# Performance work log

Measured on AMD Instinct MI355X. Metric: run time of the kernel, lower is better.

## Reference

```python
import jax, jax.numpy as jnp
import numpy as np

N = 8000        # nodes
E = 64000       # directed edges (before self-loops)
F_IN = 3201     # node_dim=1 + encoding_dim(128)*25
N_TRAIN = 4000


def setup_inputs() -> dict:
    key = jax.random.key(0)
    k = jax.random.split(key, 4)
    d = {
        'x': jax.random.normal(k[0], (N, F_IN), dtype=jnp.float32),
        'edge_index': jax.random.randint(k[1], (2, E), 0, N),
        'y': jax.random.uniform(k[2], (N,), dtype=jnp.float32),
        'train_idx': jax.random.randint(k[3], (N_TRAIN,), 0, N),
    }
    cnt = [0]
    def w(shape, fan_in):
        cnt[0] += 1
        kk = jax.random.fold_in(jax.random.key(1), cnt[0])
        return (jax.random.normal(kk, shape, dtype=jnp.float32) / np.float32(np.sqrt(fan_in)))
    ones = lambda n: jnp.ones((n,), jnp.float32)
    zeros = lambda n: jnp.zeros((n,), jnp.float32)
    d['bn0_g'] = ones(F_IN); d['bn0_b'] = zeros(F_IN)
    d['W1l'] = w((F_IN, 1024), F_IN); d['W1r'] = w((F_IN, 1024), F_IN)
    d['a1'] = w((2, 512), 512); d['b1'] = zeros(1024)
    d['bn1_g'] = ones(1024); d['bn1_b'] = zeros(1024)
    d['W2l'] = w((1024, 512), 1024); d['W2r'] = w((1024, 512), 1024)
    d['a2'] = w((1, 512), 512); d['b2'] = zeros(512)
    d['bn2_g'] = ones(512); d['bn2_b'] = zeros(512)
    d['W3l'] = w((512, 512), 512); d['W3r'] = w((512, 512), 512)
    d['a3'] = w((1, 512), 512); d['b3'] = zeros(512)
    d['bn3_g'] = ones(512); d['bn3_b'] = zeros(512)
    d['W4l'] = w((512, 512), 512); d['W4r'] = w((512, 512), 512)
    d['a4'] = w((1, 512), 512); d['b4'] = zeros(512)
    d['Wh'] = w((512, 1), 512); d['bh'] = zeros(1)
    return d


def _batchnorm(h, g, b, eps=1e-5):
    # training-mode batch statistics over the node dim
    m = h.mean(axis=0)
    v = h.var(axis=0)
    return (h - m) * jax.lax.rsqrt(v + jnp.float32(eps)) * g + b


def _gatv2(h, src, dst, Wl, Wr, att, bias, n):
    # GATv2Conv with concat heads, softmax over incoming edges, aggr='mean'
    H, C = att.shape
    xl = (h @ Wl).reshape(n, H, C)   # source transform
    xr = (h @ Wr).reshape(n, H, C)   # target transform
    z = jax.nn.leaky_relu(xl[src] + xr[dst], negative_slope=0.2)  # [E,H,C]
    e = jnp.einsum('ehc,hc->eh', z, att)                          # [E,H]
    emax = jax.ops.segment_max(e, dst, num_segments=n)            # segment softmax
    ex = jnp.exp(e - emax[dst])
    denom = jax.ops.segment_sum(ex, dst, num_segments=n)
    alpha = ex / denom[dst]
    agg = jax.ops.segment_sum(alpha[:, :, None] * xl[src], dst, num_segments=n)
    deg = jax.ops.segment_sum(jnp.ones(src.shape[0], h.dtype), dst, num_segments=n)
    return (agg / deg[:, None, None]).reshape(n, H * C) + bias


def reference(x, edge_index, y, train_idx, bn0_g, bn0_b, W1l, W1r, a1, b1,
              bn1_g, bn1_b, W2l, W2r, a2, b2, bn2_g, bn2_b, W3l, W3r, a3, b3,
              bn3_g, bn3_b, W4l, W4r, a4, b4, Wh, bh):
    n = x.shape[0]
    loops = jnp.arange(n, dtype=edge_index.dtype)  # PyG add_self_loops=True
    src = jnp.concatenate([edge_index[0], loops])
    dst = jnp.concatenate([edge_index[1], loops])
    h = _batchnorm(x, bn0_g, bn0_b)
    h = _gatv2(h, src, dst, W1l, W1r, a1, b1, n)          # -> [N,1024]
    h = jax.nn.relu(_batchnorm(h, bn1_g, bn1_b))
    h = _gatv2(h, src, dst, W2l, W2r, a2, b2, n)          # -> [N,512]
    h = jax.nn.relu(_batchnorm(h, bn2_g, bn2_b))
    h = _gatv2(h, src, dst, W3l, W3r, a3, b3, n)
    h = jax.nn.relu(_batchnorm(h, bn3_g, bn3_b))
    h = jax.nn.relu(_gatv2(h, src, dst, W4l, W4r, a4, b4, n))
    pred = jax.nn.sigmoid(h @ Wh + bh)[:, 0]              # [N]
    return pred[train_idx], y[train_idx]
```

## Files before the change

kernel.cpp:

```cpp
#include <hip/hip_runtime.h>
#include <math.h>

typedef __bf16 bf16x8 __attribute__((ext_vector_type(8)));
typedef float f32x4 __attribute__((ext_vector_type(4)));
typedef unsigned short ushort8 __attribute__((ext_vector_type(8)));

__device__ __forceinline__ float bf2f(unsigned short u) {
  union { unsigned int i; float f; } c; c.i = ((unsigned int)u) << 16; return c.f;
}
__device__ __forceinline__ unsigned short f2bf(float f) {
  union { float f; unsigned int i; } c; c.f = f;
  unsigned int r = (c.i + 0x7fffu + ((c.i >> 16) & 1u)) >> 16;
  return (unsigned short)r;
}

__global__ void zero_k(float* __restrict__ statz, int nz, int* __restrict__ deg, int n) {
  int i = blockIdx.x * blockDim.x + threadIdx.x;
  if (i < nz) statz[i] = 0.f;
  if (i < n) deg[i] = 1;
}

__global__ void deg_count_k(const int* __restrict__ dst, int* __restrict__ deg, int e) {
  int i = blockIdx.x * blockDim.x + threadIdx.x;
  if (i < e) atomicAdd(&deg[dst[i]], 1);
}

__global__ void scan_k(const int* __restrict__ deg, int* __restrict__ offsets,
                       int* __restrict__ cursor, int n) {
  __shared__ int sums[1024];
  int tid = threadIdx.x;
  int chunk = (n + 1023) >> 10;
  int base = tid * chunk;
  int s = 0;
  for (int i = 0; i < chunk; ++i) {
    int j = base + i;
    if (j < n) s += deg[j];
  }
  sums[tid] = s;
  __syncthreads();
  for (int off = 1; off < 1024; off <<= 1) {
    int v = (tid >= off) ? sums[tid - off] : 0;
    __syncthreads();
    sums[tid] += v;
    __syncthreads();
  }
  int run = sums[tid] - s;
  for (int i = 0; i < chunk; ++i) {
    int j = base + i;
    if (j < n) {
      offsets[j] = run;
      cursor[j] = run;
      run += deg[j];
    }
  }
  if (tid == 1023) offsets[n] = sums[1023];
}

__global__ void csr_fill_k(const int* __restrict__ src, const int* __restrict__ dst,
                           int* __restrict__ cursor, int* __restrict__ csr_src,
                           int e, int n) {
  int i = blockIdx.x * blockDim.x + threadIdx.x;
  if (i >= e + n) return;
  int s, d;
  if (i < e) { s = src[i]; d = dst[i]; }
  else       { s = i - e;  d = s; }
  int pos = atomicAdd(&cursor[d], 1);
  csr_src[pos] = s;
}

__global__ __launch_bounds__(256)
void stats_convert_k(const float* __restrict__ x, unsigned short* __restrict__ Abf,
                     float* __restrict__ s1, float* __restrict__ s2,
                     int M, int K, int Kp) {
  int c = blockIdx.x * 256 + threadIdx.x;
  if (c >= Kp) return;
  int rows = (M + gridDim.y - 1) / gridDim.y;
  int r0 = blockIdx.y * rows;
  int r1 = min(M, r0 + rows);
  if (c >= K) {
    for (int r = r0; r < r1; ++r) Abf[(size_t)r * Kp + c] = 0;
    return;
  }
  float a = 0.f, b = 0.f;
  int r = r0;
  for (; r + 4 <= r1; r += 4) {
    float v0 = x[(size_t)(r + 0) * K + c];
    float v1 = x[(size_t)(r + 1) * K + c];
    float v2 = x[(size_t)(r + 2) * K + c];
    float v3 = x[(size_t)(r + 3) * K + c];
    a += v0 + v1 + v2 + v3;
    b += v0 * v0 + v1 * v1 + v2 * v2 + v3 * v3;
    Abf[(size_t)(r + 0) * Kp + c] = f2bf(v0);
    Abf[(size_t)(r + 1) * Kp + c] = f2bf(v1);
    Abf[(size_t)(r + 2) * Kp + c] = f2bf(v2);
    Abf[(size_t)(r + 3) * Kp + c] = f2bf(v3);
  }
  for (; r < r1; ++r) {
    float v = x[(size_t)r * K + c];
    a += v; b += v * v;
    Abf[(size_t)r * Kp + c] = f2bf(v);
  }
  atomicAdd(&s1[c], a);
  atomicAdd(&s2[c], b);
}

__global__ __launch_bounds__(256)
void col_stats_bf_k(const unsigned short* __restrict__ h, int M, int D,
                    float* __restrict__ s1, float* __restrict__ s2) {
  int c = blockIdx.x * 256 + threadIdx.x;
  if (c >= D) return;
  int rows = (M + gridDim.y - 1) / gridDim.y;
  int r0 = blockIdx.y * rows;
  int r1 = min(M, r0 + rows);
  float a = 0.f, b = 0.f;
  int r = r0;
  for (; r + 4 <= r1; r += 4) {
    float v0 = bf2f(h[(size_t)(r + 0) * D + c]);
    float v1 = bf2f(h[(size_t)(r + 1) * D + c]);
    float v2 = bf2f(h[(size_t)(r + 2) * D + c]);
    float v3 = bf2f(h[(size_t)(r + 3) * D + c]);
    a += v0 + v1 + v2 + v3;
    b += v0 * v0 + v1 * v1 + v2 * v2 + v3 * v3;
  }
  for (; r < r1; ++r) {
    float v = bf2f(h[(size_t)r * D + c]);
    a += v; b += v * v;
  }
  atomicAdd(&s1[c], a);
  atomicAdd(&s2[c], b);
}

__global__ void bn_fin_k(const float* __restrict__ s1, const float* __restrict__ s2,
                         const float* __restrict__ g, const float* __restrict__ b,
                         float* __restrict__ acol, float* __restrict__ ccol,
                         int D, float invM) {
  int c = blockIdx.x * blockDim.x + threadIdx.x;
  if (c >= D) return;
  float m = s1[c] * invM;
  float v = fmaxf(s2[c] * invM - m * m, 0.f);
  float a = rsqrtf(v + 1e-5f) * g[c];
  acol[c] = a;
  ccol[c] = b[c] - m * a;
}

__global__ __launch_bounds__(256)
void bn_apply8_k(const unsigned short* __restrict__ h,
                 const float* __restrict__ s1, const float* __restrict__ s2,
                 const float* __restrict__ g, const float* __restrict__ b,
                 unsigned short* __restrict__ outb,
                 size_t total, int D, float invM) {
  size_t i = ((size_t)blockIdx.x * 256 + threadIdx.x) * 8;
  if (i >= total) return;
  ushort8 u = *(const ushort8*)(h + i);
  int c = (int)(i % (size_t)D);
  ushort8 o;
#pragma unroll
  for (int j = 0; j < 8; ++j) {
    float m = s1[c + j] * invM;
    float var = fmaxf(s2[c + j] * invM - m * m, 0.f);
    float a = rsqrtf(var + 1e-5f) * g[c + j];
    float cc = b[c + j] - m * a;
    float v = bf2f(u[j]) * a + cc;
    o[j] = f2bf(fmaxf(v, 0.f));
  }
  *(ushort8*)(outb + i) = o;
}

__global__ __launch_bounds__(256)
void wconv_pair_k(const float* __restrict__ Wl, const float* __restrict__ Wr,
                  unsigned short* __restrict__ WT, int K, int N, int Kp,
                  const float* __restrict__ scale, const float* __restrict__ cshift,
                  float* __restrict__ bias) {
  const float* W = blockIdx.z ? Wr : Wl;
  unsigned short* WTo = WT + (size_t)blockIdx.z * N * Kp;
  __shared__ float t[32][33];
  int n0 = blockIdx.x * 32, k0 = blockIdx.y * 32;
  int tx = threadIdx.x & 31, ty = threadIdx.x >> 5;
  float bsum = 0.f;
#pragma unroll
  for (int i = 0; i < 32; i += 8) {
    int k = k0 + ty + i, nn = n0 + tx;
    float v = (k < K && nn < N) ? W[(size_t)k * N + nn] : 0.f;
    t[ty + i][tx] = v;
    if (cshift && k < K) bsum += cshift[k] * v;
  }
  if (cshift) atomicAdd(&bias[blockIdx.z * N + n0 + tx], bsum);
  __syncthreads();
#pragma unroll
  for (int i = 0; i < 32; i += 8) {
    int nn = n0 + ty + i, k = k0 + tx;
    if (nn < N && k < Kp) {
      float v = t[tx][ty + i];
      if (scale && k < K) v *= scale[k];
      WTo[(size_t)nn * Kp + k] = f2bf(v);
    }
  }
}

__global__ __launch_bounds__(256)
void gemm_bf16_k(const unsigned short* __restrict__ A,
                 const unsigned short* __restrict__ Bt,
                 unsigned short* __restrict__ outL, unsigned short* __restrict__ outR,
                 const float* __restrict__ bias, int M, int Nh, int K) {
  __shared__ unsigned short sA[128 * 64];
  __shared__ unsigned short sB[128 * 64];
  const int tid = threadIdx.x;
  const int wave = tid >> 6, lane = tid & 63;
  const int wm = wave >> 1, wn = wave & 1;
  const int l16 = lane & 15, lq = lane >> 4;
  const int row0 = blockIdx.y * 128, col0 = blockIdx.x * 128;

  f32x4 acc[4][4] = {};

  for (int kt = 0; kt < K; kt += 64) {
#pragma unroll
    for (int i = 0; i < 4; ++i) {
      int s = i * 256 + tid;
      int r = s >> 3;
      int g = (s & 7) ^ (r & 7);
      int ra = row0 + r;
      ra = ra < M ? ra : M - 1;
      const unsigned short* ga = A + (size_t)ra * K + (kt + g * 8);
      __builtin_amdgcn_global_load_lds(
          (const __attribute__((address_space(1))) void*)ga,
          (__attribute__((address_space(3))) void*)&sA[s * 8], 16, 0, 0);
      const unsigned short* gb = Bt + (size_t)(col0 + r) * K + (kt + g * 8);
      __builtin_amdgcn_global_load_lds(
          (const __attribute__((address_space(1))) void*)gb,
          (__attribute__((address_space(3))) void*)&sB[s * 8], 16, 0, 0);
    }
    __syncthreads();
#pragma unroll
    for (int ks = 0; ks < 2; ++ks) {
      bf16x8 af[4], bff[4];
#pragma unroll
      for (int t = 0; t < 4; ++t) {
        int g = ks * 4 + lq;
        int r = wm * 64 + t * 16 + l16;
        af[t] = *(const bf16x8*)&sA[(r * 8 + (g ^ (r & 7))) * 8];
        int rb = wn * 64 + t * 16 + l16;
        bff[t] = *(const bf16x8*)&sB[(rb * 8 + (g ^ (rb & 7))) * 8];
      }
#pragma unroll
      for (int mt = 0; mt < 4; ++mt)
#pragma unroll
        for (int nt = 0; nt < 4; ++nt)
          acc[mt][nt] = __builtin_amdgcn_mfma_f32_16x16x32_bf16(af[mt], bff[nt], acc[mt][nt], 0, 0, 0);
    }
    __syncthreads();
  }
#pragma unroll
  for (int mt = 0; mt < 4; ++mt) {
    int rbase = row0 + wm * 64 + mt * 16 + lq * 4;
#pragma unroll
    for (int nt = 0; nt < 4; ++nt) {
      int col = col0 + wn * 64 + nt * 16 + l16;
      float bv = bias ? bias[col] : 0.f;
      unsigned short* base;
      int cc;
      if (col < Nh) { base = outL; cc = col; }
      else          { base = outR; cc = col - Nh; }
#pragma unroll
      for (int r = 0; r < 4; ++r) {
        int rr = rbase + r;
        if (rr < M) base[(size_t)rr * Nh + cc] = f2bf(acc[mt][nt][r] + bv);
      }
    }
  }
}

template <int H>
__global__ __launch_bounds__(256)
void gat_edge_k(const unsigned short* __restrict__ xl, const unsigned short* __restrict__ xr,
                const float* __restrict__ att, const float* __restrict__ bias,
                const int* __restrict__ csr, const int* __restrict__ offsets,
                unsigned short* __restrict__ out, int n, int relu) {
  int gw = (blockIdx.x * 256 + threadIdx.x) >> 6;
  int lane = threadIdx.x & 63;
  if (gw >= n * H) return;
  int node, head;
  if (H == 1) { node = gw; head = 0; }
  else        { node = gw >> 1; head = gw & 1; }
  const int W = H * 512;
  const size_t rowoff = (size_t)node * W + head * 512;
  const size_t choff = (size_t)head * 512 + (size_t)(lane * 8);

  float xrv[8], atv[8];
  {
    ushort8 u = *(const ushort8*)(xr + rowoff + lane * 8);
    const float* ap = att + head * 512 + lane * 8;
#pragma unroll
    for (int j = 0; j < 8; ++j) { xrv[j] = bf2f(u[j]); atv[j] = ap[j]; }
  }
  int p0 = offsets[node], p1 = offsets[node + 1];
  ushort8 u0 = *(const ushort8*)(xl + (size_t)csr[p0] * W + choff);
  ushort8 u1 = u0;
  if (p0 + 1 < p1) u1 = *(const ushort8*)(xl + (size_t)csr[p0 + 1] * W + choff);

  float m = -1e30f, l = 0.f;
  float acc[8];
#pragma unroll
  for (int j = 0; j < 8; ++j) acc[j] = 0.f;
  for (int p = p0; p < p1; ++p) {
    ushort8 u = u0;
    u0 = u1;
    if (p + 2 < p1) u1 = *(const ushort8*)(xl + (size_t)csr[p + 2] * W + choff);
    float lv[8];
    float e = 0.f;
#pragma unroll
    for (int j = 0; j < 8; ++j) {
      lv[j] = bf2f(u[j]);
      float z = lv[j] + xrv[j];
      z = fmaxf(z, 0.f) + 0.2f * fminf(z, 0.f);
      e = fmaf(z, atv[j], e);
    }
#pragma unroll
    for (int off = 32; off > 0; off >>= 1) e += __shfl_xor(e, off, 64);
    float mn = fmaxf(m, e);
    float corr = __expf(m - mn);
    float w = __expf(e - mn);
    l = l * corr + w;
#pragma unroll
    for (int j = 0; j < 8; ++j) acc[j] = acc[j] * corr + w * lv[j];
    m = mn;
  }
  float inv = 1.f / (l * (float)(p1 - p0));
  const float* bp = bias + head * 512 + lane * 8;
  ushort8 o;
#pragma unroll
  for (int j = 0; j < 8; ++j) {
    float v = acc[j] * inv + bp[j];
    if (relu) v = fmaxf(v, 0.f);
    o[j] = f2bf(v);
  }
  *(ushort8*)(out + rowoff + lane * 8) = o;
}

__global__ __launch_bounds__(256)
void head_gather_k(const unsigned short* __restrict__ h, const float* __restrict__ Wh,
                   const float* __restrict__ bh, const float* __restrict__ y,
                   const int* __restrict__ tidx, float* __restrict__ out, int nt) {
  int gw = (blockIdx.x * 256 + threadIdx.x) >> 6;
  int lane = threadIdx.x & 63;
  if (gw >= nt) return;
  int j = tidx[gw];
  ushort8 u = *(const ushort8*)(h + (size_t)j * 512 + lane * 8);
  const float* wp = Wh + lane * 8;
  float s = 0.f;
#pragma unroll
  for (int q = 0; q < 8; ++q) s = fmaf(bf2f(u[q]), wp[q], s);
#pragma unroll
  for (int off = 32; off > 0; off >>= 1) s += __shfl_xor(s, off, 64);
  if (lane == 0) {
    out[gw] = 1.f / (1.f + __expf(-(s + bh[0])));
    out[nt + gw] = y[j];
  }
}

extern "C" void kernel_launch(void* const* d_in, const int* in_sizes, int n_in,
                              void* d_out, int out_size, void* d_ws, size_t ws_size,
                              hipStream_t stream) {
  const float* x     = (const float*)d_in[0];
  const int*   ei    = (const int*)d_in[1];
  const float* y     = (const float*)d_in[2];
  const int*   tidx  = (const int*)d_in[3];
  const float* bn0_g = (const float*)d_in[4];
  const float* bn0_b = (const float*)d_in[5];
  const float* W1l   = (const float*)d_in[6];
  const float* W1r   = (const float*)d_in[7];
  const float* a1    = (const float*)d_in[8];
  const float* b1    = (const float*)d_in[9];
  const float* bn1_g = (const float*)d_in[10];
  const float* bn1_b = (const float*)d_in[11];
  const float* W2l   = (const float*)d_in[12];
  const float* W2r   = (const float*)d_in[13];
  const float* a2    = (const float*)d_in[14];
  const float* b2    = (const float*)d_in[15];
  const float* bn2_g = (const float*)d_in[16];
  const float* bn2_b = (const float*)d_in[17];
  const float* W3l   = (const float*)d_in[18];
  const float* W3r   = (const float*)d_in[19];
  const float* a3    = (const float*)d_in[20];
  const float* b3    = (const float*)d_in[21];
  const float* bn3_g = (const float*)d_in[22];
  const float* bn3_b = (const float*)d_in[23];
  const float* W4l   = (const float*)d_in[24];
  const float* W4r   = (const float*)d_in[25];
  const float* a4    = (const float*)d_in[26];
  const float* b4    = (const float*)d_in[27];
  const float* Wh    = (const float*)d_in[28];
  const float* bh    = (const float*)d_in[29];
  float* out = (float*)d_out;

  const int n   = in_sizes[2];
  const int E   = in_sizes[1] / 2;
  const int FIN = in_sizes[4];
  const int NT  = in_sizes[3];
  const int ET  = E + n;
  const int KP1 = 3264;

  unsigned short* us = (unsigned short*)d_ws;
  const size_t ABF_SZ = (size_t)n * KP1;
  unsigned short* Abf = us;
  unsigned short* hb  = us + ABF_SZ;
  unsigned short* xlb = hb + (size_t)n * 1024;
  unsigned short* xrb = xlb + (size_t)n * 1024;
  float* fp = (float*)(xrb + (size_t)n * 1024);
  float* s1_0  = fp;           fp += 3328;
  float* s2_0  = fp;           fp += 3328;
  float* s1_1  = fp;           fp += 1024;
  float* s2_1  = fp;           fp += 1024;
  float* s1_2  = fp;           fp += 1024;
  float* s2_2  = fp;           fp += 1024;
  float* s1_3  = fp;           fp += 1024;
  float* s2_3  = fp;           fp += 1024;
  float* biasb = fp;           fp += 2048;
  const int kZeroCount = 14848;
  float* acol  = fp;           fp += 3328;
  float* ccol  = fp;           fp += 3328;
  int* deg     = (int*)fp;
  int* offsets = deg + n;
  int* cursor  = offsets + n + 1;
  int* csr     = cursor + n;
  unsigned short* W1T = hb;
  unsigned short* WT  = Abf + (size_t)n * 1024;

  zero_k<<<(kZeroCount + 255) / 256, 256, 0, stream>>>(s1_0, kZeroCount, deg, n);
  deg_count_k<<<(E + 255) / 256, 256, 0, stream>>>(ei + E, deg, E);
  scan_k<<<1, 1024, 0, stream>>>(deg, offsets, cursor, n);
  csr_fill_k<<<(ET + 255) / 256, 256, 0, stream>>>(ei, ei + E, cursor, csr, E, n);

  float invM = 1.f / (float)n;

  {
    dim3 g((KP1 + 255) / 256, 200);
    stats_convert_k<<<g, 256, 0, stream>>>(x, Abf, s1_0, s2_0, n, FIN, KP1);
    bn_fin_k<<<(FIN + 255) / 256, 256, 0, stream>>>(s1_0, s2_0, bn0_g, bn0_b, acol, ccol, FIN, invM);
  }

  {
    dim3 gw1(1024 / 32, KP1 / 32, 2);
    wconv_pair_k<<<gw1, 256, 0, stream>>>(W1l, W1r, W1T, FIN, 1024, KP1, acol, ccol, biasb);
    dim3 g(2048 / 128, (n + 127) / 128);
    gemm_bf16_k<<<g, 256, 0, stream>>>(Abf, W1T, xlb, xrb, biasb, n, 1024, KP1);
  }
  gat_edge_k<2><<<(n * 2 + 3) / 4, 256, 0, stream>>>(xlb, xrb, a1, b1, csr, offsets, hb, n, 0);
  {
    dim3 g(1024 / 256, 160);
    col_stats_bf_k<<<g, 256, 0, stream>>>(hb, n, 1024, s1_1, s2_1);
    bn_apply8_k<<<(int)(((size_t)n * 1024 / 8 + 255) / 256), 256, 0, stream>>>(
        hb, s1_1, s2_1, bn1_g, bn1_b, Abf, (size_t)n * 1024, 1024, invM);
  }

  {
    dim3 gw2(512 / 32, 1024 / 32, 2);
    wconv_pair_k<<<gw2, 256, 0, stream>>>(W2l, W2r, WT, 1024, 512, 1024, nullptr, nullptr, nullptr);
    dim3 g(1024 / 128, (n + 127) / 128);
    gemm_bf16_k<<<g, 256, 0, stream>>>(Abf, WT, xlb, xrb, nullptr, n, 512, 1024);
  }
  gat_edge_k<1><<<(n + 3) / 4, 256, 0, stream>>>(xlb, xrb, a2, b2, csr, offsets, hb, n, 0);
  {
    dim3 g(512 / 256, 160);
    col_stats_bf_k<<<g, 256, 0, stream>>>(hb, n, 512, s1_2, s2_2);
    bn_apply8_k<<<(int)(((size_t)n * 512 / 8 + 255) / 256), 256, 0, stream>>>(
        hb, s1_2, s2_2, bn2_g, bn2_b, Abf, (size_t)n * 512, 512, invM);
  }

  {
    dim3 gw3(512 / 32, 512 / 32, 2);
    wconv_pair_k<<<gw3, 256, 0, stream>>>(W3l, W3r, WT, 512, 512, 512, nullptr, nullptr, nullptr);
    dim3 g(1024 / 128, (n + 127) / 128);
    gemm_bf16_k<<<g, 256, 0, stream>>>(Abf, WT, xlb, xrb, nullptr, n, 512, 512);
  }
  gat_edge_k<1><<<(n + 3) / 4, 256, 0, stream>>>(xlb, xrb, a3, b3, csr, offsets, hb, n, 0);
  {
    dim3 g(512 / 256, 160);
    col_stats_bf_k<<<g, 256, 0, stream>>>(hb, n, 512, s1_3, s2_3);
    bn_apply8_k<<<(int)(((size_t)n * 512 / 8 + 255) / 256), 256, 0, stream>>>(
        hb, s1_3, s2_3, bn3_g, bn3_b, Abf, (size_t)n * 512, 512, invM);
  }

  {
    dim3 gw4(512 / 32, 512 / 32, 2);
    wconv_pair_k<<<gw4, 256, 0, stream>>>(W4l, W4r, WT, 512, 512, 512, nullptr, nullptr, nullptr);
    dim3 g(1024 / 128, (n + 127) / 128);
    gemm_bf16_k<<<g, 256, 0, stream>>>(Abf, WT, xlb, xrb, nullptr, n, 512, 512);
  }
  gat_edge_k<1><<<(n + 3) / 4, 256, 0, stream>>>(xlb, xrb, a4, b4, csr, offsets, hb, n, 1);

  head_gather_k<<<(NT + 3) / 4, 256, 0, stream>>>(hb, Wh, bh, y, tidx, out, NT);
}
```

Before: 837.1 us.

## Fuse BN finalize into weight conversion, XCD-aware GEMM tile remap, deeper edge prefetch

Drops the separate bn_fin_k launch by computing per-column BN scale and shift inside wconv_pair_k straight from the accumulated sums. Remaps GEMM block indices so consecutive column tiles land on the same XCD, to improve L2 reuse of the B operand on MI355X's multi-die layout. Deepens the gather prefetch in the GAT edge kernel from two to three rows ahead to hide more latency. The cost is redundant rsqrt work per block and more registers in the edge kernel.

```diff
diff --git a/kernel.cpp b/kernel.cpp
--- a/kernel.cpp
+++ b/kernel.cpp
@@ -130,19 +130,6 @@
   atomicAdd(&s2[c], b);
 }
 
-__global__ void bn_fin_k(const float* __restrict__ s1, const float* __restrict__ s2,
-                         const float* __restrict__ g, const float* __restrict__ b,
-                         float* __restrict__ acol, float* __restrict__ ccol,
-                         int D, float invM) {
-  int c = blockIdx.x * blockDim.x + threadIdx.x;
-  if (c >= D) return;
-  float m = s1[c] * invM;
-  float v = fmaxf(s2[c] * invM - m * m, 0.f);
-  float a = rsqrtf(v + 1e-5f) * g[c];
-  acol[c] = a;
-  ccol[c] = b[c] - m * a;
-}
-
 __global__ __launch_bounds__(256)
 void bn_apply8_k(const unsigned short* __restrict__ h,
                  const float* __restrict__ s1, const float* __restrict__ s2,
@@ -169,8 +156,9 @@
 __global__ __launch_bounds__(256)
 void wconv_pair_k(const float* __restrict__ Wl, const float* __restrict__ Wr,
                   unsigned short* __restrict__ WT, int K, int N, int Kp,
-                  const float* __restrict__ scale, const float* __restrict__ cshift,
-                  float* __restrict__ bias) {
+                  const float* __restrict__ s1, const float* __restrict__ s2,
+                  const float* __restrict__ gg, const float* __restrict__ bb,
+                  float* __restrict__ bias, float invM) {
   const float* W = blockIdx.z ? Wr : Wl;
   unsigned short* WTo = WT + (size_t)blockIdx.z * N * Kp;
   __shared__ float t[32][33];
@@ -182,16 +170,30 @@
     int k = k0 + ty + i, nn = n0 + tx;
     float v = (k < K && nn < N) ? W[(size_t)k * N + nn] : 0.f;
     t[ty + i][tx] = v;
-    if (cshift && k < K) bsum += cshift[k] * v;
-  }
-  if (cshift) atomicAdd(&bias[blockIdx.z * N + n0 + tx], bsum);
+    if (s1 && k < K) {
+      float m = s1[k] * invM;
+      float var = fmaxf(s2[k] * invM - m * m, 0.f);
+      float a = rsqrtf(var + 1e-5f) * gg[k];
+      float c = bb[k] - m * a;
+      bsum += c * v;
+    }
+  }
+  if (s1) atomicAdd(&bias[blockIdx.z * N + n0 + tx], bsum);
+  float ascale = 1.f;
+  if (s1) {
+    int k = k0 + tx;
+    if (k < K) {
+      float m = s1[k] * invM;
+      float var = fmaxf(s2[k] * invM - m * m, 0.f);
+      ascale = rsqrtf(var + 1e-5f) * gg[k];
+    }
+  }
   __syncthreads();
 #pragma unroll
   for (int i = 0; i < 32; i += 8) {
     int nn = n0 + ty + i, k = k0 + tx;
     if (nn < N && k < Kp) {
-      float v = t[tx][ty + i];
-      if (scale && k < K) v *= scale[k];
+      float v = t[tx][ty + i] * ascale;
       WTo[(size_t)nn * Kp + k] = f2bf(v);
     }
   }
@@ -208,7 +210,21 @@
   const int wave = tid >> 6, lane = tid & 63;
   const int wm = wave >> 1, wn = wave & 1;
   const int l16 = lane & 15, lq = lane >> 4;
-  const int row0 = blockIdx.y * 128, col0 = blockIdx.x * 128;
+
+  int ct, rt;
+  {
+    int bid = blockIdx.y * gridDim.x + blockIdx.x;
+    int nb = gridDim.x * gridDim.y;
+    if (((nb & 7) == 0) && ((gridDim.x & 7) == 0)) {
+      int cpx = gridDim.x >> 3;
+      int xcd = bid & 7, j = bid >> 3;
+      ct = xcd * cpx + (j & (cpx - 1));
+      rt = j / cpx;
+    } else {
+      ct = blockIdx.x; rt = blockIdx.y;
+    }
+  }
+  const int row0 = rt * 128, col0 = ct * 128;
 
   f32x4 acc[4][4] = {};
 
@@ -294,8 +310,9 @@
   }
   int p0 = offsets[node], p1 = offsets[node + 1];
   ushort8 u0 = *(const ushort8*)(xl + (size_t)csr[p0] * W + choff);
-  ushort8 u1 = u0;
+  ushort8 u1 = u0, u2 = u0;
   if (p0 + 1 < p1) u1 = *(const ushort8*)(xl + (size_t)csr[p0 + 1] * W + choff);
+  if (p0 + 2 < p1) u2 = *(const ushort8*)(xl + (size_t)csr[p0 + 2] * W + choff);
 
   float m = -1e30f, l = 0.f;
   float acc[8];
@@ -303,8 +320,8 @@
   for (int j = 0; j < 8; ++j) acc[j] = 0.f;
   for (int p = p0; p < p1; ++p) {
     ushort8 u = u0;
-    u0 = u1;
-    if (p + 2 < p1) u1 = *(const ushort8*)(xl + (size_t)csr[p + 2] * W + choff);
+    u0 = u1; u1 = u2;
+    if (p + 3 < p1) u2 = *(const ushort8*)(xl + (size_t)csr[p + 3] * W + choff);
     float lv[8];
     float e = 0.f;
 #pragma unroll
@@ -416,8 +433,6 @@
   float* s2_3  = fp;           fp += 1024;
   float* biasb = fp;           fp += 2048;
   const int kZeroCount = 14848;
-  float* acol  = fp;           fp += 3328;
-  float* ccol  = fp;           fp += 3328;
   int* deg     = (int*)fp;
   int* offsets = deg + n;
   int* cursor  = offsets + n + 1;
@@ -435,12 +450,12 @@
   {
     dim3 g((KP1 + 255) / 256, 200);
     stats_convert_k<<<g, 256, 0, stream>>>(x, Abf, s1_0, s2_0, n, FIN, KP1);
-    bn_fin_k<<<(FIN + 255) / 256, 256, 0, stream>>>(s1_0, s2_0, bn0_g, bn0_b, acol, ccol, FIN, invM);
   }
 
   {
     dim3 gw1(1024 / 32, KP1 / 32, 2);
-    wconv_pair_k<<<gw1, 256, 0, stream>>>(W1l, W1r, W1T, FIN, 1024, KP1, acol, ccol, biasb);
+    wconv_pair_k<<<gw1, 256, 0, stream>>>(W1l, W1r, W1T, FIN, 1024, KP1,
+                                          s1_0, s2_0, bn0_g, bn0_b, biasb, invM);
     dim3 g(2048 / 128, (n + 127) / 128);
     gemm_bf16_k<<<g, 256, 0, stream>>>(Abf, W1T, xlb, xrb, biasb, n, 1024, KP1);
   }
@@ -454,7 +469,8 @@
 
   {
     dim3 gw2(512 / 32, 1024 / 32, 2);
-    wconv_pair_k<<<gw2, 256, 0, stream>>>(W2l, W2r, WT, 1024, 512, 1024, nullptr, nullptr, nullptr);
+    wconv_pair_k<<<gw2, 256, 0, stream>>>(W2l, W2r, WT, 1024, 512, 1024,
+                                          nullptr, nullptr, nullptr, nullptr, nullptr, 0.f);
     dim3 g(1024 / 128, (n + 127) / 128);
     gemm_bf16_k<<<g, 256, 0, stream>>>(Abf, WT, xlb, xrb, nullptr, n, 512, 1024);
   }
@@ -468,7 +484,8 @@
 
   {
     dim3 gw3(512 / 32, 512 / 32, 2);
-    wconv_pair_k<<<gw3, 256, 0, stream>>>(W3l, W3r, WT, 512, 512, 512, nullptr, nullptr, nullptr);
+    wconv_pair_k<<<gw3, 256, 0, stream>>>(W3l, W3r, WT, 512, 512, 512,
+                                          nullptr, nullptr, nullptr, nullptr, nullptr, 0.f);
     dim3 g(1024 / 128, (n + 127) / 128);
     gemm_bf16_k<<<g, 256, 0, stream>>>(Abf, WT, xlb, xrb, nullptr, n, 512, 512);
   }
@@ -482,7 +499,8 @@
 
   {
     dim3 gw4(512 / 32, 512 / 32, 2);
-    wconv_pair_k<<<gw4, 256, 0, stream>>>(W4l, W4r, WT, 512, 512, 512, nullptr, nullptr, nullptr);
+    wconv_pair_k<<<gw4, 256, 0, stream>>>(W4l, W4r, WT, 512, 512, 512,
+                                          nullptr, nullptr, nullptr, nullptr, nullptr, 0.f);
     dim3 g(1024 / 128, (n + 127) / 128);
     gemm_bf16_k<<<g, 256, 0, stream>>>(Abf, WT, xlb, xrb, nullptr, n, 512, 512);
   }
```

New measurement: 843.9 us. Within noise of the previous version (+0.8%).
